# Performance work log

Measured on AMD Instinct MI355X. Metric: run time of the kernel, lower is better.

Reference implementation:

```python
import jax, jax.numpy as jnp
import numpy as np

B, S, D, H = 4, 2048, 1024, 16
HS = D // H  # head_size = 64
EPS = 1e-5


def setup_inputs() -> dict:
    key = jax.random.key(0)
    ks = jax.random.split(key, 10)
    s = 0.02
    return {
        "v": jax.random.normal(ks[0], (B, S, D), dtype=jnp.float32),
        "k": jax.random.normal(ks[1], (B, S, D), dtype=jnp.float32),
        "q": jax.random.normal(ks[2], (B, S, D), dtype=jnp.float32),
        "mask": jnp.triu(jnp.ones((S, S), dtype=bool), k=1),  # True = masked (causal)
        "ln_g": jnp.ones((D,), dtype=jnp.float32),
        "ln_b": jnp.zeros((D,), dtype=jnp.float32),
        # per-head projections, stacked: [H, D, HS]
        "Wq": jax.random.normal(ks[3], (H, D, HS), dtype=jnp.float32) * s,
        "Wk": jax.random.normal(ks[4], (H, D, HS), dtype=jnp.float32) * s,
        "Wv": jax.random.normal(ks[5], (H, D, HS), dtype=jnp.float32) * s,
        "Wp": jax.random.normal(ks[6], (D, D), dtype=jnp.float32) * s,
        "bp": jnp.zeros((D,), dtype=jnp.float32),
    }


def _layernorm(x, g, b):
    mu = jnp.mean(x, axis=-1, keepdims=True)
    var = jnp.var(x, axis=-1, keepdims=True)
    return (x - mu) * jax.lax.rsqrt(var + EPS) * g + b


def reference(v, k, q, mask, ln_g, ln_b, Wq, Wk, Wv, Wp, bp):
    v = _layernorm(v, ln_g, ln_b)
    k = _layernorm(k, ln_g, ln_b)
    q = _layernorm(q, ln_g, ln_b)
    # per-head projections: [B,S,D] x [H,D,E] -> [B,H,S,E]
    qh = jnp.einsum("bsd,hde->bhse", q, Wq)
    kh = jnp.einsum("bsd,hde->bhse", k, Wk)
    vh = jnp.einsum("bsd,hde->bhse", v, Wv)
    # NOTE: original scales by full embedding_dim C**-0.5 (not head_size)
    scale = jnp.float32(D) ** -0.5
    w = jnp.einsum("bhqe,bhke->bhqk", qh, kh) * scale
    w = jnp.where(mask, -jnp.inf, w)
    w = jax.nn.softmax(w, axis=-1)
    out = jnp.einsum("bhqk,bhke->bhqe", w, vh)  # [B,H,S,E]
    out = out.transpose(0, 2, 1, 3).reshape(B, S, D)  # concat heads
    return out @ Wp.T + bp
```

## Files before the change

kernel.cpp:

```cpp
#include <hip/hip_runtime.h>
#include <hip/hip_bf16.h>
#include <cstdint>
#include <cstddef>

#define Bq 4
#define Sq 2048
#define Dq 1024
#define Hq 16
#define HSq 64
#define Kc 1024

typedef short short8 __attribute__((ext_vector_type(8)));
typedef float f32x4 __attribute__((ext_vector_type(4)));

__device__ __forceinline__ unsigned short f2bf(float f){
  __hip_bfloat16 h = __float2bfloat16(f);
  return __builtin_bit_cast(unsigned short, h);
}

__device__ __forceinline__ float exp2hw(float x){
  float r;
  asm("v_exp_f32 %0, %1" : "=v"(r) : "v"(x));
  return r;
}
__device__ __forceinline__ unsigned cvtpk(float lo, float hi){
  unsigned r;
  asm("v_cvt_pk_bf16_f32 %0, %1, %2" : "=v"(r) : "v"(lo), "v"(hi));
  return r;
}
__device__ __forceinline__ float rcphw(float x){
  float r;
  asm("v_rcp_f32 %0, %1" : "=v"(r) : "v"(x));
  return r;
}

__device__ __forceinline__ void gl_lds16(const void* g, void* l){
  __builtin_amdgcn_global_load_lds((const __attribute__((address_space(1))) void*)(g),
                                   (__attribute__((address_space(3))) void*)(l), 16, 0, 0);
}

__global__ __launch_bounds__(256) void prep_kernel(
    const float* __restrict__ v, const float* __restrict__ k, const float* __restrict__ q,
    const float* __restrict__ g, const float* __restrict__ bta,
    const float* __restrict__ Wq, const float* __restrict__ Wk, const float* __restrict__ Wv,
    const float* __restrict__ Wp,
    short* __restrict__ vo, short* __restrict__ ko, short* __restrict__ qo,
    short* __restrict__ wqt, short* __restrict__ wkt, short* __restrict__ wvt,
    short* __restrict__ wpb)
{
  const int bid = blockIdx.x;
  const int t = threadIdx.x;

  if (bid < 24576){
    const int which = bid >> 13;
    const int row   = bid & 8191;
    const float* x = (which==0) ? v : (which==1) ? k : q;
    short* out     = (which==0) ? vo : (which==1) ? ko : qo;
    const float* xr = x + (size_t)row * Dq;
    float4 vv = reinterpret_cast<const float4*>(xr)[t];
    float s  = vv.x + vv.y + vv.z + vv.w;
    float ss = vv.x*vv.x + vv.y*vv.y + vv.z*vv.z + vv.w*vv.w;
    #pragma unroll
    for (int o = 32; o >= 1; o >>= 1){ s += __shfl_xor(s, o); ss += __shfl_xor(ss, o); }
    __shared__ float red[8];
    const int wid = t >> 6;
    if ((t & 63) == 0){ red[wid] = s; red[4+wid] = ss; }
    __syncthreads();
    s  = red[0]+red[1]+red[2]+red[3];
    ss = red[4]+red[5]+red[6]+red[7];
    const float mu   = s * (1.0f/Dq);
    const float var  = ss * (1.0f/Dq) - mu*mu;
    const float rstd = rsqrtf(var + 1e-5f);
    float4 gv = reinterpret_cast<const float4*>(g)[t];
    float4 bv = reinterpret_cast<const float4*>(bta)[t];
    ushort4 o4;
    o4.x = f2bf((vv.x-mu)*rstd*gv.x + bv.x);
    o4.y = f2bf((vv.y-mu)*rstd*gv.y + bv.y);
    o4.z = f2bf((vv.z-mu)*rstd*gv.z + bv.z);
    o4.w = f2bf((vv.w-mu)*rstd*gv.w + bv.w);
    reinterpret_cast<ushort4*>(out + (size_t)row*Dq)[t] = o4;
  } else if (bid < 25344){
    const int idx = bid - 24576;
    const int z   = idx >> 8;
    const int rem = idx & 255;
    const int h   = rem >> 4;
    const int kt  = rem & 15;
    const float* Wsrc = (z==0) ? Wq : (z==1) ? Wk : Wv;
    short* Wdst       = (z==0) ? wqt : (z==1) ? wkt : wvt;
    const float scl   = (z==0) ? (0.03125f * 1.44269504f) : 1.0f;
    __shared__ short tb[64][68];
    const float* src = Wsrc + ((size_t)h*Kc + (size_t)kt*64) * HSq;
    #pragma unroll
    for (int c=0;c<4;c++){
      int lin = c*256 + t;
      int kr = lin >> 4;
      int e4 = (lin & 15) * 4;
      float4 vv = *reinterpret_cast<const float4*>(&src[(size_t)kr*HSq + e4]);
      tb[e4+0][kr] = (short)f2bf(vv.x*scl);
      tb[e4+1][kr] = (short)f2bf(vv.y*scl);
      tb[e4+2][kr] = (short)f2bf(vv.z*scl);
      tb[e4+3][kr] = (short)f2bf(vv.w*scl);
    }
    __syncthreads();
    short* dst = Wdst + (size_t)h*HSq*Kc + (size_t)kt*64;
    #pragma unroll
    for (int c=0;c<4;c++){
      int lin = c*256 + t;
      int er = lin >> 4;
      int k4 = (lin & 15) * 4;
      ushort4 o;
      o.x = (unsigned short)tb[er][k4+0];
      o.y = (unsigned short)tb[er][k4+1];
      o.z = (unsigned short)tb[er][k4+2];
      o.w = (unsigned short)tb[er][k4+3];
      *reinterpret_cast<ushort4*>(&dst[(size_t)er*Kc + k4]) = o;
    }
  } else {
    int i = (bid - 25344)*256 + t;
    float4 vv = reinterpret_cast<const float4*>(Wp)[i];
    ushort4 o; o.x=f2bf(vv.x); o.y=f2bf(vv.y); o.z=f2bf(vv.z); o.w=f2bf(vv.w);
    reinterpret_cast<ushort4*>(wpb)[i] = o;
  }
}

__global__ __launch_bounds__(512, 2) void proj3_kernel(
    const short* __restrict__ qn, const short* __restrict__ kn, const short* __restrict__ vn,
    const short* __restrict__ wqt, const short* __restrict__ wkt, const short* __restrict__ wvt,
    short* __restrict__ qh, short* __restrict__ kh, short* __restrict__ vhT)
{
  const int z = blockIdx.y;
  const short* A  = (z==0) ? qn  : (z==1) ? kn  : vn;
  const short* BT = (z==0) ? wqt : (z==1) ? wkt : wvt;

  const int i = blockIdx.x;
  const int bm = i & 31, bn = i >> 5;
  const int m0 = bm * 256;
  const int n0c = bn * 256;
  const int tid = threadIdx.x;
  const int lane = tid & 63, w = tid >> 6;
  const int wm = w >> 2, wn = w & 3;
  const int fr = lane & 15, fg = lane >> 4;

  __shared__ short As[2*256*64];
  __shared__ short Bs[2*256*64];

  f32x4 acc[8][4] = {};
  short8 bf[4][2];

  const int srow = tid >> 3;
  const int sw   = ((tid & 7) << 4) ^ ((srow & 7) << 4);
  const char* aB = (const char*)(A  + (size_t)(m0  + srow)*Kc) + sw;
  const char* bB = (const char*)(BT + (size_t)(n0c + srow)*Kc) + sw;

#define STAGE(t, hh, buf) do{                                              \
    const bool isB_ = (hh) < 2;                                            \
    const char* s_ = (isB_ ? bB : aB) + (size_t)((hh)&1)*(128*2048) + (size_t)(t)*128; \
    char* d_ = (char*)(isB_ ? (void*)Bs : (void*)As) + (buf)*32768 + ((hh)&1)*16384 + w*1024; \
    gl_lds16(s_, d_);                                                      \
    gl_lds16(s_ + 64*2048, d_ + 8192);                                     \
  }while(0)

#define READ_A(p, buf, af) do{                                             \
    _Pragma("unroll") for (int mm=0; mm<2; ++mm){                          \
      const int r_ = ((p)*2+mm)*32 + wm*16 + fr;                           \
      _Pragma("unroll") for (int kk=0; kk<2; ++kk){                        \
        const int byt_ = (buf)*32768 + r_*128 + (((kk*4+fg)^(r_&7))<<4);   \
        af[mm][kk] = *reinterpret_cast<const short8*>((const char*)As + byt_); \
      }}}while(0)

#define MFMA_P(p, af) do{                                                  \
    __builtin_amdgcn_s_setprio(1);                                         \
    _Pragma("unroll") for (int kk=0; kk<2; ++kk)                           \
      _Pragma("unroll") for (int mm=0; mm<2; ++mm)                         \
        _Pragma("unroll") for (int nr=0; nr<4; ++nr)                       \
          acc[(p)*2+mm][nr] = __builtin_amdgcn_mfma_f32_16x16x32_bf16(af[mm][kk], bf[nr][kk], acc[(p)*2+mm][nr], 0, 0, 0); \
    __builtin_amdgcn_s_setprio(0);                                         \
  }while(0)

#define DO_TILE(t, buf, HN) do{                                            \
    asm volatile("s_waitcnt vmcnt(2)" ::: "memory");                       \
    __builtin_amdgcn_s_barrier();                                          \
    _Pragma("unroll") for (int nr=0; nr<4; ++nr){                          \
      const int r_ = wn*64 + nr*16 + fr;                                   \
      _Pragma("unroll") for (int kk=0; kk<2; ++kk){                        \
        const int byt_ = (buf)*32768 + r_*128 + (((kk*4+fg)^(r_&7))<<4);   \
        bf[nr][kk] = *reinterpret_cast<const short8*>((const char*)Bs + byt_); \
      }}                                                                   \
    { short8 af[2][2]; READ_A(0, buf, af);                                 \
      if (HN) STAGE((t)+1, 0, (buf)^1);                                    \
      MFMA_P(0, af); }                                                     \
    { short8 af[2][2]; READ_A(1, buf, af);                                 \
      if (HN) STAGE((t)+1, 1, (buf)^1);                                    \
      MFMA_P(1, af); }                                                     \
    if (HN) { asm volatile("s_waitcnt vmcnt(4)" ::: "memory"); }           \
    else    { asm volatile("s_waitcnt vmcnt(0)" ::: "memory"); }           \
    __builtin_amdgcn_s_barrier();                                          \
    { short8 af[2][2]; READ_A(2, buf, af);                                 \
      if (HN) STAGE((t)+1, 2, (buf)^1);                                    \
      MFMA_P(2, af); }                                                     \
    { short8 af[2][2]; READ_A(3, buf, af);                                 \
      if (HN) STAGE((t)+1, 3, (buf)^1);                                    \
      MFMA_P(3, af); }                                                     \
  }while(0)

  STAGE(0, 0, 0); STAGE(0, 1, 0); STAGE(0, 2, 0); STAGE(0, 3, 0);

  for (int t2 = 0; t2 < 7; ++t2){
    const int t = t2*2;
    DO_TILE(t,   0, true);
    DO_TILE(t+1, 1, true);
  }
  DO_TILE(14, 0, true);
  DO_TILE(15, 1, false);

#undef DO_TILE
#undef MFMA_P
#undef READ_A
#undef STAGE

  if (z == 2){
    #pragma unroll
    for (int mi=0; mi<8; ++mi){
      #pragma unroll
      for (int nr=0; nr<4; ++nr){
        int col = n0c + wn*64 + nr*16 + fr;
        int h = col >> 6, e = col & 63;
        int R = m0 + mi*32 + wm*16 + fg*4;
        int bb = R >> 11, sPos = R & (Sq-1);
        uint2 o;
        o.x = cvtpk(acc[mi][nr][0], acc[mi][nr][1]);
        o.y = cvtpk(acc[mi][nr][2], acc[mi][nr][3]);
        *reinterpret_cast<uint2*>(&vhT[(((size_t)bb*Hq + h)*HSq + e)*Sq + sPos]) = o;
      }
    }
  } else {
    short* outb = z ? kh : qh;
    #pragma unroll
    for (int mi=0; mi<8; ++mi){
      #pragma unroll
      for (int nr=0; nr<4; ++nr){
        int col = n0c + wn*64 + nr*16 + fr;
        int h = col >> 6, e = col & 63;
        #pragma unroll
        for (int r=0; r<4; ++r){
          int R = m0 + mi*32 + wm*16 + fg*4 + r;
          int bb = R >> 11, sPos = R & (Sq-1);
          outb[(((size_t)bb*Hq + h)*Sq + sPos)*HSq + e] = (short)f2bf(acc[mi][nr][r]);
        }
      }
    }
  }
}

__global__ __launch_bounds__(256) void gemmo_kernel(
    const short* __restrict__ A,
    const short* __restrict__ BT,
    const float* __restrict__ bias,
    float* __restrict__ outf)
{
  const int bid = blockIdx.x;
  const int c8_ = bid & 7, j = bid >> 3;
  const int bm = c8_*8 + (j & 7), bn = j >> 3;
  const int m0 = bm * 128;
  const int n0c = bn * 128;
  const int tid = threadIdx.x;
  const int lane = tid & 63, w = tid >> 6;
  const int wm = w >> 1, wn = w & 1;
  const int fr = lane & 15, fg = lane >> 4;

  __shared__ short As[128*64];
  __shared__ short Bs[128*64];

  f32x4 acc[4][4] = {};

  const int rowT = tid >> 3;
  const int inb  = (tid & 7) * 16;

  for (int kt = 0; kt < Kc/64; ++kt){
    const int k0 = kt*64;
    #pragma unroll
    for (int c=0;c<4;c++){
      int row = c*32 + rowT;
      int src = inb ^ ((row & 7) << 4);
      gl_lds16((const char*)(A  + (size_t)(m0  + row)*Kc + k0) + src,
               (char*)As + c*4096 + w*1024);
      gl_lds16((const char*)(BT + (size_t)(n0c + row)*Kc + k0) + src,
               (char*)Bs + c*4096 + w*1024);
    }
    __syncthreads();
    #pragma unroll
    for (int kk=0;kk<2;kk++){
      short8 af[4], bf8[4];
      #pragma unroll
      for (int mr=0;mr<4;mr++){
        int row = wm*64 + mr*16 + fr;
        int byt = row*128 + ((kk*64 + fg*16) ^ ((row & 7) << 4));
        af[mr] = *reinterpret_cast<const short8*>((const char*)As + byt);
      }
      #pragma unroll
      for (int nr=0;nr<4;nr++){
        int row = wn*64 + nr*16 + fr;
        int byt = row*128 + ((kk*64 + fg*16) ^ ((row & 7) << 4));
        bf8[nr] = *reinterpret_cast<const short8*>((const char*)Bs + byt);
      }
      #pragma unroll
      for (int mr=0;mr<4;mr++)
        #pragma unroll
        for (int nr=0;nr<4;nr++)
          acc[mr][nr] = __builtin_amdgcn_mfma_f32_16x16x32_bf16(af[mr], bf8[nr], acc[mr][nr], 0, 0, 0);
    }
    __syncthreads();
  }

  #pragma unroll
  for (int mr=0;mr<4;mr++){
    #pragma unroll
    for (int nr=0;nr<4;nr++){
      int col = n0c + wn*64 + nr*16 + fr;
      #pragma unroll
      for (int r=0;r<4;r++){
        int R = m0 + wm*64 + mr*16 + fg*4 + r;
        outf[(size_t)R*Dq + col] = acc[mr][nr][r] + bias[col];
      }
    }
  }
}

__global__ __launch_bounds__(256, 4) void attn_kernel(
    const short* __restrict__ qh, const short* __restrict__ kh,
    const short* __restrict__ vhT, short* __restrict__ attO)
{
  const int bid = blockIdx.x;
  const int jp  = bid >> 6;
  const int g   = bid & 63;
  const int h = g & 15, b = g >> 4;
  const short* Q  = qh  + (((size_t)b*Hq + h)*Sq)*HSq;
  const short* K  = kh  + (((size_t)b*Hq + h)*Sq)*HSq;
  const short* VT = vhT + (((size_t)b*Hq + h)*HSq)*Sq;
  const int tid = threadIdx.x, w = tid >> 6, lane = tid & 63;
  const int fr = lane & 15, fg = lane >> 4;

  __shared__ short KsB[2][64*64];
  __shared__ short VtB[2][64*64];
  __shared__ short Ps[4][32][76];

  const int sRow = tid >> 3;
  const int swz  = ((tid & 7) << 4) ^ ((sRow & 7) << 4);
  const char* pK = (const char*)K  + (size_t)sRow*128      + swz;
  const char* pV = (const char*)VT + (size_t)sRow*(Sq*2)   + swz;

  short8 ones;
  #pragma unroll
  for (int ii=0;ii<8;ii++) ones[ii] = (short)0x3F80;

  for (int pass = 0; pass < 2; ++pass){
    const int qt = pass ? jp : (15 - jp);
    const int qbase = qt * 128;
    const int nkv = 2*qt + 2;

    short8 qa[2][2];
    #pragma unroll
    for (int mr=0;mr<2;mr++){
      const int qrow = qbase + w*32 + mr*16 + fr;
      #pragma unroll
      for (int kk=0;kk<2;kk++)
        qa[mr][kk] = *reinterpret_cast<const short8*>(&Q[(size_t)qrow*HSq + kk*32 + 8*fg]);
    }

    f32x4 accO[2][4] = {};
    f32x4 accL[2] = {};

    #pragma unroll
    for (int c=0;c<2;c++){
      gl_lds16(pK + c*4096,   (char*)KsB[0] + c*4096 + w*1024);
      gl_lds16(pV + c*131072, (char*)VtB[0] + c*4096 + w*1024);
    }
    __syncthreads();

    for (int kt0 = 0; kt0 < nkv; kt0 += 2){
      #pragma unroll
      for (int u = 0; u < 2; ++u){
        const int kt = kt0 + u;
        const int buf = u;

        if (kt+1 < nkv){
          const char* nK = pK + (size_t)(kt+1)*8192;
          const char* nV = pV + (size_t)(kt+1)*128;
          #pragma unroll
          for (int c=0;c<2;c++){
            gl_lds16(nK + c*4096,   (char*)KsB[buf^1] + c*4096 + w*1024);
            gl_lds16(nV + c*131072, (char*)VtB[buf^1] + c*4096 + w*1024);
          }
        }

        f32x4 sfr[2][4] = {};
        __builtin_amdgcn_s_setprio(1);
        #pragma unroll
        for (int kk=0;kk<2;kk++){
          short8 kb[4];
          #pragma unroll
          for (int n0=0;n0<4;n0++){
            int row = n0*16 + fr;
            int byt = row*128 + ((((kk*4+fg) ^ (row & 7))) << 4);
            kb[n0] = *reinterpret_cast<const short8*>((const char*)KsB[buf] + byt);
          }
          #pragma unroll
          for (int mr=0;mr<2;mr++)
            #pragma unroll
            for (int n0=0;n0<4;n0++)
              sfr[mr][n0] = __builtin_amdgcn_mfma_f32_16x16x32_bf16(kb[n0], qa[mr][kk], sfr[mr][n0], 0, 0, 0);
        }
        __builtin_amdgcn_s_setprio(0);

        #pragma unroll
        for (int mr=0;mr<2;mr++){
          const int qr = qbase + w*32 + mr*16 + fr;
          const bool needmask = (kt*64 + 63) > (qbase + w*32 + mr*16);
          #pragma unroll
          for (int n0=0;n0<4;n0++){
            float p0 = exp2hw(sfr[mr][n0][0]);
            float p1 = exp2hw(sfr[mr][n0][1]);
            float p2 = exp2hw(sfr[mr][n0][2]);
            float p3 = exp2hw(sfr[mr][n0][3]);
            if (needmask){
              int kc = kt*64 + n0*16 + fg*4;
              if (kc+0 > qr) p0 = 0.0f;
              if (kc+1 > qr) p1 = 0.0f;
              if (kc+2 > qr) p2 = 0.0f;
              if (kc+3 > qr) p3 = 0.0f;
            }
            uint2 u2;
            u2.x = cvtpk(p0, p1);
            u2.y = cvtpk(p2, p3);
            *reinterpret_cast<uint2*>(&Ps[w][mr*16 + fr][n0*16 + fg*4]) = u2;
          }
        }

        __builtin_amdgcn_s_setprio(1);
        #pragma unroll
        for (int kk=0;kk<2;kk++){
          short8 pa[2], vb[4];
          #pragma unroll
          for (int mr=0;mr<2;mr++)
            pa[mr] = *reinterpret_cast<short8*>(&Ps[w][mr*16 + fr][kk*32 + 8*fg]);
          #pragma unroll
          for (int n0=0;n0<4;n0++){
            int row = n0*16 + fr;
            int byt = row*128 + ((((kk*4+fg) ^ (row & 7))) << 4);
            vb[n0] = *reinterpret_cast<const short8*>((const char*)VtB[buf] + byt);
          }
          #pragma unroll
          for (int mr=0;mr<2;mr++){
            #pragma unroll
            for (int n0=0;n0<4;n0++)
              accO[mr][n0] = __builtin_amdgcn_mfma_f32_16x16x32_bf16(vb[n0], pa[mr], accO[mr][n0], 0, 0, 0);
            accL[mr] = __builtin_amdgcn_mfma_f32_16x16x32_bf16(ones, pa[mr], accL[mr], 0, 0, 0);
          }
        }
        __builtin_amdgcn_s_setprio(0);

        __syncthreads();
      }
    }

    #pragma unroll
    for (int mr=0;mr<2;mr++){
      float inv = rcphw(accL[mr][0]);
      const int qr = qbase + w*32 + mr*16 + fr;
      short* orow = attO + ((size_t)b*Sq + qr)*Dq + h*HSq;
      #pragma unroll
      for (int n0=0;n0<4;n0++){
        uint2 u2;
        u2.x = cvtpk(accO[mr][n0][0] * inv, accO[mr][n0][1] * inv);
        u2.y = cvtpk(accO[mr][n0][2] * inv, accO[mr][n0][3] * inv);
        *reinterpret_cast<uint2*>(&orow[n0*16 + fg*4]) = u2;
      }
    }
  }
}

extern "C" void kernel_launch(void* const* d_in, const int* in_sizes, int n_in,
                              void* d_out, int out_size, void* d_ws, size_t ws_size,
                              hipStream_t stream){
  const float* v_in = (const float*)d_in[0];
  const float* k_in = (const float*)d_in[1];
  const float* q_in = (const float*)d_in[2];
  const float* ln_g = (const float*)d_in[4];
  const float* ln_b = (const float*)d_in[5];
  const float* Wq   = (const float*)d_in[6];
  const float* Wk   = (const float*)d_in[7];
  const float* Wv   = (const float*)d_in[8];
  const float* Wp   = (const float*)d_in[9];
  const float* bp   = (const float*)d_in[10];
  float* out = (float*)d_out;

  char* ws = (char*)d_ws;
  const size_t BSD  = (size_t)Bq*Sq*Dq;
  const size_t BSD2 = BSD * 2;
  short* vn  = (short*)(ws);
  short* kn  = (short*)(ws + BSD2);
  short* qn  = (short*)(ws + 2*BSD2);
  short* wqt = (short*)(ws + 3*BSD2);
  short* wkt = (short*)(ws + 3*BSD2 + 2097152);
  short* wvt = (short*)(ws + 3*BSD2 + 2*2097152);
  short* wpb = (short*)(ws + 3*BSD2 + 3*2097152);
  short* qh  = (short*)(ws + 3*BSD2 + 4*2097152);
  short* kh  = qh + BSD;
  short* vhT = kh + BSD;
  short* attO = vn;

  prep_kernel<<<26368, 256, 0, stream>>>(v_in, k_in, q_in, ln_g, ln_b,
                                         Wq, Wk, Wv, Wp,
                                         vn, kn, qn, wqt, wkt, wvt, wpb);

  proj3_kernel<<<dim3(128, 3), 512, 0, stream>>>(qn, kn, vn, wqt, wkt, wvt, qh, kh, vhT);

  attn_kernel<<<512, 256, 0, stream>>>(qh, kh, vhT, attO);

  gemmo_kernel<<<512, 256, 0, stream>>>(attO, wpb, bp, out);
}
```

Baseline: 178.1 us.

## Use 1024-thread blocks in projection GEMM with half the accumulators per wave

```diff
diff --git a/kernel.cpp b/kernel.cpp
--- a/kernel.cpp
+++ b/kernel.cpp
@@ -123,7 +123,7 @@
   }
 }
 
-__global__ __launch_bounds__(512, 2) void proj3_kernel(
+__global__ __launch_bounds__(1024, 1) void proj3_kernel(
     const short* __restrict__ qn, const short* __restrict__ kn, const short* __restrict__ vn,
     const short* __restrict__ wqt, const short* __restrict__ wkt, const short* __restrict__ wvt,
     short* __restrict__ qh, short* __restrict__ kh, short* __restrict__ vhT)
@@ -144,7 +144,7 @@
   __shared__ short As[2*256*64];
   __shared__ short Bs[2*256*64];
 
-  f32x4 acc[8][4] = {};
+  f32x4 acc[4][4] = {};
   short8 bf[4][2];
 
   const int srow = tid >> 3;
@@ -157,28 +157,25 @@
     const char* s_ = (isB_ ? bB : aB) + (size_t)((hh)&1)*(128*2048) + (size_t)(t)*128; \
     char* d_ = (char*)(isB_ ? (void*)Bs : (void*)As) + (buf)*32768 + ((hh)&1)*16384 + w*1024; \
     gl_lds16(s_, d_);                                                      \
-    gl_lds16(s_ + 64*2048, d_ + 8192);                                     \
   }while(0)
 
 #define READ_A(p, buf, af) do{                                             \
-    _Pragma("unroll") for (int mm=0; mm<2; ++mm){                          \
-      const int r_ = ((p)*2+mm)*32 + wm*16 + fr;                           \
-      _Pragma("unroll") for (int kk=0; kk<2; ++kk){                        \
-        const int byt_ = (buf)*32768 + r_*128 + (((kk*4+fg)^(r_&7))<<4);   \
-        af[mm][kk] = *reinterpret_cast<const short8*>((const char*)As + byt_); \
-      }}}while(0)
+    const int r_ = (p)*64 + wm*16 + fr;                                    \
+    _Pragma("unroll") for (int kk=0; kk<2; ++kk){                          \
+      const int byt_ = (buf)*32768 + r_*128 + (((kk*4+fg)^(r_&7))<<4);     \
+      af[kk] = *reinterpret_cast<const short8*>((const char*)As + byt_);   \
+    }}while(0)
 
 #define MFMA_P(p, af) do{                                                  \
     __builtin_amdgcn_s_setprio(1);                                         \
     _Pragma("unroll") for (int kk=0; kk<2; ++kk)                           \
-      _Pragma("unroll") for (int mm=0; mm<2; ++mm)                         \
-        _Pragma("unroll") for (int nr=0; nr<4; ++nr)                       \
-          acc[(p)*2+mm][nr] = __builtin_amdgcn_mfma_f32_16x16x32_bf16(af[mm][kk], bf[nr][kk], acc[(p)*2+mm][nr], 0, 0, 0); \
+      _Pragma("unroll") for (int nr=0; nr<4; ++nr)                         \
+        acc[(p)][nr] = __builtin_amdgcn_mfma_f32_16x16x32_bf16(af[kk], bf[nr][kk], acc[(p)][nr], 0, 0, 0); \
     __builtin_amdgcn_s_setprio(0);                                         \
   }while(0)
 
 #define DO_TILE(t, buf, HN) do{                                            \
-    asm volatile("s_waitcnt vmcnt(2)" ::: "memory");                       \
+    asm volatile("s_waitcnt vmcnt(1)" ::: "memory");                       \
     __builtin_amdgcn_s_barrier();                                          \
     _Pragma("unroll") for (int nr=0; nr<4; ++nr){                          \
       const int r_ = wn*64 + nr*16 + fr;                                   \
@@ -186,19 +183,19 @@
         const int byt_ = (buf)*32768 + r_*128 + (((kk*4+fg)^(r_&7))<<4);   \
         bf[nr][kk] = *reinterpret_cast<const short8*>((const char*)Bs + byt_); \
       }}                                                                   \
-    { short8 af[2][2]; READ_A(0, buf, af);                                 \
+    { short8 af[2]; READ_A(0, buf, af);                                    \
       if (HN) STAGE((t)+1, 0, (buf)^1);                                    \
       MFMA_P(0, af); }                                                     \
-    { short8 af[2][2]; READ_A(1, buf, af);                                 \
+    { short8 af[2]; READ_A(1, buf, af);                                    \
       if (HN) STAGE((t)+1, 1, (buf)^1);                                    \
       MFMA_P(1, af); }                                                     \
-    if (HN) { asm volatile("s_waitcnt vmcnt(4)" ::: "memory"); }           \
+    if (HN) { asm volatile("s_waitcnt vmcnt(2)" ::: "memory"); }           \
     else    { asm volatile("s_waitcnt vmcnt(0)" ::: "memory"); }           \
     __builtin_amdgcn_s_barrier();                                          \
-    { short8 af[2][2]; READ_A(2, buf, af);                                 \
+    { short8 af[2]; READ_A(2, buf, af);                                    \
       if (HN) STAGE((t)+1, 2, (buf)^1);                                    \
       MFMA_P(2, af); }                                                     \
-    { short8 af[2][2]; READ_A(3, buf, af);                                 \
+    { short8 af[2]; READ_A(3, buf, af);                                    \
       if (HN) STAGE((t)+1, 3, (buf)^1);                                    \
       MFMA_P(3, af); }                                                     \
   }while(0)
@@ -220,32 +217,32 @@
 
   if (z == 2){
     #pragma unroll
-    for (int mi=0; mi<8; ++mi){
+    for (int p=0; p<4; ++p){
       #pragma unroll
       for (int nr=0; nr<4; ++nr){
         int col = n0c + wn*64 + nr*16 + fr;
         int h = col >> 6, e = col & 63;
-        int R = m0 + mi*32 + wm*16 + fg*4;
+        int R = m0 + p*64 + wm*16 + fg*4;
         int bb = R >> 11, sPos = R & (Sq-1);
         uint2 o;
-        o.x = cvtpk(acc[mi][nr][0], acc[mi][nr][1]);
-        o.y = cvtpk(acc[mi][nr][2], acc[mi][nr][3]);
+        o.x = cvtpk(acc[p][nr][0], acc[p][nr][1]);
+        o.y = cvtpk(acc[p][nr][2], acc[p][nr][3]);
         *reinterpret_cast<uint2*>(&vhT[(((size_t)bb*Hq + h)*HSq + e)*Sq + sPos]) = o;
       }
     }
   } else {
     short* outb = z ? kh : qh;
     #pragma unroll
-    for (int mi=0; mi<8; ++mi){
+    for (int p=0; p<4; ++p){
       #pragma unroll
       for (int nr=0; nr<4; ++nr){
         int col = n0c + wn*64 + nr*16 + fr;
         int h = col >> 6, e = col & 63;
         #pragma unroll
         for (int r=0; r<4; ++r){
-          int R = m0 + mi*32 + wm*16 + fg*4 + r;
+          int R = m0 + p*64 + wm*16 + fg*4 + r;
           int bb = R >> 11, sPos = R & (Sq-1);
-          outb[(((size_t)bb*Hq + h)*Sq + sPos)*HSq + e] = (short)f2bf(acc[mi][nr][r]);
+          outb[(((size_t)bb*Hq + h)*Sq + sPos)*HSq + e] = (short)f2bf(acc[p][nr][r]);
         }
       }
     }
@@ -513,7 +510,7 @@
                                          Wq, Wk, Wv, Wp,
                                          vn, kn, qn, wqt, wkt, wvt, wpb);
 
-  proj3_kernel<<<dim3(128, 3), 512, 0, stream>>>(qn, kn, vn, wqt, wkt, wvt, qh, kh, vhT);
+  proj3_kernel<<<dim3(128, 3), 1024, 0, stream>>>(qn, kn, vn, wqt, wkt, wvt, qh, kh, vhT);
 
   attn_kernel<<<512, 256, 0, stream>>>(qh, kh, vhT, attO);
 
```

New measurement: 176.7 us. About the same (-0.8%).
